# Kernel tuning notes

Hardware: AMD Instinct MI355X
Metric: run time of the kernel (lower is better)

Reference implementation:

```python
import jax, jax.numpy as jnp
import numpy as np

K = 4
HEADS = 4
IN_F = 128
OUT_F = 256
OUT_H = OUT_F // HEADS  # 64


def setup_inputs() -> dict:
    key = jax.random.key(0)
    ks = jax.random.split(key, 6)
    B, N = 8, 2048
    x = jax.random.normal(ks[0], (B, N, IN_F), dtype=jnp.float32)
    adj = jax.random.uniform(ks[1], (B, N, N), dtype=jnp.float32)
    # per-head linear: weight [H, out_h, in_f*(K+1)], bias [H, out_h]
    w_heads = 0.01 * jax.random.normal(ks[2], (HEADS, OUT_H, IN_F * (K + 1)), dtype=jnp.float32)
    b_heads = 0.01 * jax.random.normal(ks[3], (HEADS, OUT_H), dtype=jnp.float32)
    # final linear: [OUT_F, OUT_F]
    w_out = 0.01 * jax.random.normal(ks[4], (OUT_F, OUT_F), dtype=jnp.float32)
    b_out = 0.01 * jax.random.normal(ks[5], (OUT_F,), dtype=jnp.float32)
    return {"x": x, "adj": adj, "w_heads": w_heads, "b_heads": b_heads,
            "w_out": w_out, "b_out": b_out}


def _normalized_adj(adj):
    B, N, _ = adj.shape
    A_hat = adj + jnp.eye(N, dtype=adj.dtype)
    d = jnp.sum(A_hat, axis=2) ** -0.5          # [B, N]
    # L_hat = D^-1/2 A_hat D^-1/2 (diag scaling, no dense diag matmuls)
    return d[:, :, None] * A_hat * d[:, None, :]


def _legendre_stack(L, K):
    # elementwise Legendre recurrence on L; returns [B, N, N, K+1]
    P = [jnp.ones_like(L), L]
    for k in range(2, K + 1):
        P.append(((2 * k - 1) * L * P[-1] - (k - 1) * P[-2]) / k)
    return jnp.stack(P, axis=-1)


def reference(x, adj, w_heads, b_heads, w_out, b_out):
    B, N, F = x.shape
    L_hat = _normalized_adj(adj)                 # [B, N, N]
    LP = _legendre_stack(L_hat, K)               # [B, N, N, K+1] (shared by heads)
    # per-k propagation: cat([LP_k @ x for k], dim=2) -> k-major feature order
    prop = jnp.einsum('bnmk,bmf->bnkf', LP, x)   # [B, N, K+1, F]
    prop = prop.reshape(B, N, (K + 1) * F)       # [B, N, (K+1)*F]
    # per-head linear, concat heads along last dim (head-major)
    hout = jnp.einsum('bnc,hoc->bnho', prop, w_heads) + b_heads  # [B, N, H, out_h]
    hout = hout.reshape(B, N, HEADS * OUT_H)     # [B, N, OUT_F]
    return hout @ w_out.T + b_out                # [B, N, OUT_F]
```

## Files before the change

kernel.cpp:

```cpp
#include <hip/hip_runtime.h>
#include <hip/hip_bf16.h>
#include <stdint.h>

#define BATCH 8
#define NN    2048
#define FF    128
#define OUTF  256
#define C14   512

typedef unsigned short u16;
typedef u16  u16x8 __attribute__((ext_vector_type(8)));
typedef float f32x4 __attribute__((ext_vector_type(4)));

__device__ __forceinline__ u16 f2bf(float x) {
    union { float f; uint32_t u; } v; v.f = x;
    uint32_t r = v.u + 0x7FFFu + ((v.u >> 16) & 1u);
    return (u16)(r >> 16);
}
__device__ __forceinline__ uint32_t pk2(float a, float b) {
    __hip_bfloat162 h = __float22bfloat162_rn(make_float2(a, b));
    union { __hip_bfloat162 h; uint32_t u; } cv; cv.h = h; return cv.u;
}

__device__ __forceinline__ f32x4 mfma_bf16(u16x8 a, u16x8 b, f32x4 c) {
    asm("v_mfma_f32_16x16x32_bf16 %0, %1, %2, %0" : "+v"(c) : "v"(a), "v"(b));
    return c;
}

__global__ __launch_bounds__(256) void k_rowsum(const float* __restrict__ adj,
                                                float* __restrict__ dv) {
    size_t row = blockIdx.x;
    const float4* p = (const float4*)(adj + row * NN);
    int t = threadIdx.x;
    float4 v0 = p[t], v1 = p[t + 256];
    float s = v0.x + v0.y + v0.z + v0.w + v1.x + v1.y + v1.z + v1.w;
    #pragma unroll
    for (int off = 32; off > 0; off >>= 1) s += __shfl_down(s, off);
    __shared__ float r4[4];
    if ((t & 63) == 0) r4[t >> 6] = s;
    __syncthreads();
    if (t == 0) dv[row] = rsqrtf(r4[0] + r4[1] + r4[2] + r4[3] + 1.0f);
}

__global__ __launch_bounds__(256) void k_xprep(const float* __restrict__ x,
                                               u16* __restrict__ xT,
                                               float* __restrict__ part) {
    __shared__ u16 tile[FF][66];
    __shared__ float red[256];
    int b = blockIdx.x >> 5, mt = blockIdx.x & 31;
    const float* xb = x + ((size_t)(b * NN) + mt * 64) * FF;
    int t = threadIdx.x;
    float s = 0.f;
    #pragma unroll
    for (int i = 0; i < 32; ++i) {
        int idx = i * 256 + t;
        int ml = idx >> 7, f = idx & 127;
        float v = xb[idx];
        tile[f][ml] = f2bf(v);
        s += v;
    }
    red[t] = s;
    __syncthreads();
    u16* xb2 = xT + (size_t)b * FF * NN + mt * 64;
    #pragma unroll
    for (int i = 0; i < 16; ++i) {
        int p = i * 256 + t;
        int f = p >> 5, mp = p & 31;
        uint32_t v = (uint32_t)tile[f][2 * mp] | ((uint32_t)tile[f][2 * mp + 1] << 16);
        *(uint32_t*)(xb2 + (size_t)f * NN + 2 * mp) = v;
    }
    if (t < 128) part[(size_t)blockIdx.x * FF + t] = red[t] + red[t + 128];
}

__global__ __launch_bounds__(256) void k_weff(const float* __restrict__ wh,
                                              const float* __restrict__ wo,
                                              float* __restrict__ weff0,
                                              u16* __restrict__ w14) {
    int o = blockIdx.x, t = threadIdx.x;
    __shared__ float wrow[256];
    wrow[t] = wo[o * 256 + t];
    __syncthreads();
    int c2 = (t < 128) ? (t + 512) : 639;
    float s0 = 0.f, s1 = 0.f, s2 = 0.f;
    for (int i = 0; i < 256; ++i) {
        float w = wrow[i];
        const float* row = wh + (size_t)i * 640;
        s0 = fmaf(w, row[t], s0);
        s1 = fmaf(w, row[t + 256], s1);
        s2 = fmaf(w, row[c2], s2);
    }
    if (t < 128) weff0[o * 128 + t] = s0;
    else         w14[(size_t)o * C14 + (t - 128)] = f2bf(s0);
    w14[(size_t)o * C14 + (t + 128)] = f2bf(s1);
    if (t < 128) w14[(size_t)o * C14 + (t + 384)] = f2bf(s2);
}

__global__ __launch_bounds__(256) void k_cb(const float* __restrict__ part,
                                            const float* __restrict__ weff0,
                                            const float* __restrict__ wo,
                                            const float* __restrict__ bh,
                                            const float* __restrict__ bo,
                                            float* __restrict__ cb) {
    int b = blockIdx.x, t = threadIdx.x;
    __shared__ float cs[128];
    __shared__ float bhl[256];
    if (t < 128) {
        float s = 0.f;
        for (int j = 0; j < 32; ++j) s += part[(size_t)(b * 32 + j) * FF + t];
        cs[t] = s;
    }
    bhl[t] = bh[t];
    __syncthreads();
    float s = bo[t];
    for (int i = 0; i < 256; ++i) s = fmaf(wo[(size_t)t * 256 + i], bhl[i], s);
    for (int f = 0; f < 128; ++f) s = fmaf(weff0[t * 128 + f], cs[f], s);
    cb[b * 256 + t] = s;
}

struct MRegs { u16x8 bv[4]; f32x4 av[2]; f32x4 dmv; };

__device__ __forceinline__ void m_prefetch(MRegs& R, const u16* xTb, const float* adjb,
                                           const float* dvb, int mbase, int tid) {
    #pragma unroll
    for (int it = 0; it < 4; ++it) {
        int ci = it * 256 + tid; int f = ci >> 3, c = ci & 7;
        R.bv[it] = *(const u16x8*)(xTb + (size_t)f * NN + mbase + c * 8);
    }
    int q = tid & 15;
    R.dmv = *(const f32x4*)(dvb + mbase + q * 4);
    #pragma unroll
    for (int i = 0; i < 2; ++i) {
        int r = i * 16 + (tid >> 4);
        R.av[i] = *(const f32x4*)(adjb + (size_t)r * NN + mbase + q * 4);
    }
}

__device__ __forceinline__ void m_commit(const MRegs& R, u16* Ab, u16* Bb,
                                         const float* dn_l, int mbase, int rt, int tid) {
    #pragma unroll
    for (int it = 0; it < 4; ++it) {
        int ci = it * 256 + tid; int f = ci >> 3, c = ci & 7;
        *(u16x8*)((char*)Bb + f * 128 + ((c ^ (f & 7)) << 4)) = R.bv[it];
    }
    int q = tid & 15;
    #pragma unroll
    for (int i = 0; i < 2; ++i) {
        int r = i * 16 + (tid >> 4);
        int ng = rt * 32 + r - mbase - q * 4;
        float dnv = dn_l[r];
        float L[4], P2[4], P3[4], P4[4];
        #pragma unroll
        for (int j = 0; j < 4; ++j) {
            float a = R.av[i][j] + ((j == ng) ? 1.f : 0.f);
            L[j]  = a * dnv * R.dmv[j];
            P2[j] = fmaf(1.5f * L[j], L[j], -0.5f);
            P3[j] = L[j] * fmaf(1.66666667f, P2[j], -0.66666667f);
            P4[j] = fmaf(1.75f * L[j], P3[j], -0.75f * P2[j]);
        }
        char* base = (char*)Ab + (uint32_t)(r * 128 + ((q * 8) ^ ((r & 7) << 4)));
        *(uint2*)(base)         = make_uint2(pk2(L[0],  L[1]),  pk2(L[2],  L[3]));
        *(uint2*)(base + 4096)  = make_uint2(pk2(P2[0], P2[1]), pk2(P2[2], P2[3]));
        *(uint2*)(base + 8192)  = make_uint2(pk2(P3[0], P3[1]), pk2(P3[2], P3[3]));
        *(uint2*)(base + 12288) = make_uint2(pk2(P4[0], P4[1]), pk2(P4[2], P4[3]));
    }
}

__device__ __forceinline__ void m_mfma(const u16* A, const u16* B, int lane, f32x4 acc[2][8]) {
    #pragma unroll
    for (int kk = 0; kk < 2; ++kk) {
        int ch = (kk << 2) + (lane >> 4);
        u16x8 af[2];
        #pragma unroll
        for (int mi = 0; mi < 2; ++mi) {
            int row = mi * 16 + (lane & 15);
            af[mi] = *(const u16x8*)((const char*)A + row * 128 + ((ch ^ (row & 7)) << 4));
        }
        #pragma unroll
        for (int ni = 0; ni < 8; ++ni) {
            int fr = ni * 16 + (lane & 15);
            u16x8 bf = *(const u16x8*)((const char*)B + fr * 128 + ((ch ^ (fr & 7)) << 4));
            acc[0][ni] = mfma_bf16(af[0], bf, acc[0][ni]);
            acc[1][ni] = mfma_bf16(af[1], bf, acc[1][ni]);
        }
    }
}

__global__ __launch_bounds__(256, 2) void k_main(const float* __restrict__ adj,
                                                 const float* __restrict__ dvec,
                                                 const u16* __restrict__ xT,
                                                 u16* __restrict__ prop) {
    __shared__ __align__(16) u16 Abuf[2][4 * 32 * 64];
    __shared__ __align__(16) u16 Bbuf[2][FF * 64];
    __shared__ float dn_l[32];

    int tid = threadIdx.x, lane = tid & 63, wv = tid >> 6;
    int bb = blockIdx.x >> 6, rt = blockIdx.x & 63;
    const float* adjb = adj + (size_t)bb * NN * NN + (size_t)(rt * 32) * NN;
    const float* dvb = dvec + bb * NN;
    const u16* xTb = xT + (size_t)bb * FF * NN;

    f32x4 acc[2][8];
    #pragma unroll
    for (int mi = 0; mi < 2; ++mi)
        #pragma unroll
        for (int ni = 0; ni < 8; ++ni) acc[mi][ni] = (f32x4){0.f, 0.f, 0.f, 0.f};

    MRegs R0, R1;
    if (tid < 32) dn_l[tid] = dvec[bb * NN + rt * 32 + tid];
    m_prefetch(R0, xTb, adjb, dvb, 0, tid);
    __syncthreads();
    m_commit(R0, Abuf[0], Bbuf[0], dn_l, 0, rt, tid);
    m_prefetch(R1, xTb, adjb, dvb, 64, tid);
    __syncthreads();

    for (int ks = 0; ks < 32; ks += 2) {
        if (ks + 2 < 32) m_prefetch(R0, xTb, adjb, dvb, (ks + 2) * 64, tid);
        m_commit(R1, Abuf[1], Bbuf[1], dn_l, (ks + 1) * 64, rt, tid);
        m_mfma((const u16*)Abuf[0] + wv * 2048, (const u16*)Bbuf[0], lane, acc);
        __syncthreads();
        if (ks + 3 < 32) m_prefetch(R1, xTb, adjb, dvb, (ks + 3) * 64, tid);
        if (ks + 2 < 32) m_commit(R0, Abuf[0], Bbuf[0], dn_l, (ks + 2) * 64, rt, tid);
        m_mfma((const u16*)Abuf[1] + wv * 2048, (const u16*)Bbuf[1], lane, acc);
        __syncthreads();
    }
    asm volatile("s_nop 15\n\ts_nop 15");
    u16* pb = prop + ((size_t)bb * NN + rt * 32) * C14 + wv * 128;
    #pragma unroll
    for (int mi = 0; mi < 2; ++mi)
        #pragma unroll
        for (int ni = 0; ni < 8; ++ni) {
            int col = ni * 16 + (lane & 15);
            #pragma unroll
            for (int r4 = 0; r4 < 4; ++r4) {
                int row = mi * 16 + ((lane >> 4) << 2) + r4;
                pb[(size_t)row * C14 + col] = f2bf(acc[mi][ni][r4]);
            }
        }
}

struct FRegs { u16x8 a; u16x8 b[8]; };

__device__ __forceinline__ void f_prefetch(FRegs& R, const u16* Ap, const u16* w14,
                                           int mb, int tid) {
    { int r = tid >> 3, c = tid & 7;
      R.a = *(const u16x8*)(Ap + (size_t)r * C14 + mb + c * 8); }
    #pragma unroll
    for (int it = 0; it < 8; ++it) {
        int ci = it * 256 + tid; int o = ci >> 3, c = ci & 7;
        R.b[it] = *(const u16x8*)(w14 + (size_t)o * C14 + mb + c * 8);
    }
}
__device__ __forceinline__ void f_commit(const FRegs& R, u16* FA, u16* FB, int tid) {
    { int r = tid >> 3, c = tid & 7;
      *(u16x8*)((char*)FA + r * 128 + ((c ^ (r & 7)) << 4)) = R.a; }
    #pragma unroll
    for (int it = 0; it < 8; ++it) {
        int ci = it * 256 + tid; int o = ci >> 3, c = ci & 7;
        *(u16x8*)((char*)FB + o * 128 + ((c ^ (o & 7)) << 4)) = R.b[it];
    }
}
__device__ __forceinline__ void f_mfma(const u16* FA, const u16* FB, int lane, int wv,
                                       f32x4 acc[2][4]) {
    #pragma unroll
    for (int kk = 0; kk < 2; ++kk) {
        int ch = (kk << 2) + (lane >> 4);
        u16x8 af[2];
        #pragma unroll
        for (int mi = 0; mi < 2; ++mi) {
            int row = mi * 16 + (lane & 15);
            af[mi] = *(const u16x8*)((const char*)FA + row * 128 + ((ch ^ (row & 7)) << 4));
        }
        #pragma unroll
        for (int ni = 0; ni < 4; ++ni) {
            int o = wv * 64 + ni * 16 + (lane & 15);
            u16x8 bf = *(const u16x8*)((const char*)FB + o * 128 + ((ch ^ (o & 7)) << 4));
            acc[0][ni] = mfma_bf16(af[0], bf, acc[0][ni]);
            acc[1][ni] = mfma_bf16(af[1], bf, acc[1][ni]);
        }
    }
}

__global__ __launch_bounds__(256, 2) void k_final(const u16* __restrict__ prop,
                                                  const u16* __restrict__ w14,
                                                  const float* __restrict__ cb,
                                                  float* __restrict__ out) {
    __shared__ __align__(16) u16 FA[2][32 * 64];
    __shared__ __align__(16) u16 FB[2][256 * 64];
    int tid = threadIdx.x, lane = tid & 63, wv = tid >> 6;
    int rt = blockIdx.x, bb = rt >> 6;
    const u16* Ap = prop + (size_t)rt * 32 * C14;

    f32x4 acc[2][4];
    #pragma unroll
    for (int mi = 0; mi < 2; ++mi)
        #pragma unroll
        for (int ni = 0; ni < 4; ++ni) acc[mi][ni] = (f32x4){0.f, 0.f, 0.f, 0.f};

    FRegs R0, R1;
    f_prefetch(R0, Ap, w14, 0, tid);
    f_commit(R0, FA[0], FB[0], tid);
    f_prefetch(R1, Ap, w14, 64, tid);
    __syncthreads();

    for (int ks = 0; ks < 8; ks += 2) {
        if (ks + 2 < 8) f_prefetch(R0, Ap, w14, (ks + 2) * 64, tid);
        f_commit(R1, FA[1], FB[1], tid);
        f_mfma(FA[0], FB[0], lane, wv, acc);
        __syncthreads();
        if (ks + 3 < 8) f_prefetch(R1, Ap, w14, (ks + 3) * 64, tid);
        if (ks + 2 < 8) f_commit(R0, FA[0], FB[0], tid);
        f_mfma(FA[1], FB[1], lane, wv, acc);
        __syncthreads();
    }
    asm volatile("s_nop 15\n\ts_nop 15");
    float* ob = out + (size_t)rt * 32 * OUTF;
    const float* cbb = cb + bb * OUTF + wv * 64;
    #pragma unroll
    for (int mi = 0; mi < 2; ++mi)
        #pragma unroll
        for (int ni = 0; ni < 4; ++ni) {
            int col = ni * 16 + (lane & 15);
            float cv = cbb[col];
            #pragma unroll
            for (int r4 = 0; r4 < 4; ++r4) {
                int row = mi * 16 + ((lane >> 4) << 2) + r4;
                ob[(size_t)row * OUTF + wv * 64 + col] = acc[mi][ni][r4] + cv;
            }
        }
}

extern "C" void kernel_launch(void* const* d_in, const int* in_sizes, int n_in,
                              void* d_out, int out_size, void* d_ws, size_t ws_size,
                              hipStream_t stream) {
    const float* x   = (const float*)d_in[0];
    const float* adj = (const float*)d_in[1];
    const float* wh  = (const float*)d_in[2];
    const float* bh  = (const float*)d_in[3];
    const float* wo  = (const float*)d_in[4];
    const float* bo  = (const float*)d_in[5];

    char* p = (char*)d_ws;
    float* dvec  = (float*)p;  p += (size_t)BATCH * NN * 4;
    u16*   xT    = (u16*)p;    p += (size_t)BATCH * FF * NN * 2;
    float* part  = (float*)p;  p += (size_t)256 * FF * 4;
    float* weff0 = (float*)p;  p += (size_t)OUTF * FF * 4;
    u16*   w14   = (u16*)p;    p += (size_t)OUTF * C14 * 2;
    float* cbv   = (float*)p;  p += (size_t)BATCH * OUTF * 4;
    u16*   prop  = (u16*)p;    p += (size_t)BATCH * NN * C14 * 2;

    k_rowsum<<<dim3(BATCH * NN), dim3(256), 0, stream>>>(adj, dvec);
    k_xprep <<<dim3(256),        dim3(256), 0, stream>>>(x, xT, part);
    k_weff  <<<dim3(256),        dim3(256), 0, stream>>>(wh, wo, weff0, w14);
    k_cb    <<<dim3(BATCH),      dim3(256), 0, stream>>>(part, weff0, wo, bh, bo, cbv);
    k_main  <<<dim3(512),        dim3(256), 0, stream>>>(adj, dvec, xT, prop);
    k_final <<<dim3(512),        dim3(256), 0, stream>>>(prop, w14, cbv, (float*)d_out);
}
```

Measured before the change: 304.8 us.

## Fuse propagation and output GEMM kernels; merge x-prep and weight-fold kernels

Merges k_xprep and k_weff into one k_prep launch that splits work by block index. Fuses k_main and k_final into k_mf, so each block computes its 32-row propagation tile, writes it to a per-block scratch in global memory, then reads it back to run the output GEMM with the same shared-memory pool reused. This removes two launches and the gap between the propagation and final stages, and the reread tile is likely still in cache. The fused kernel's shared memory grows to 72KB, which could limit occupancy, and the intermediate still round-trips through global memory.

```diff
diff --git a/kernel.cpp b/kernel.cpp
--- a/kernel.cpp
+++ b/kernel.cpp
@@ -21,7 +21,6 @@
     __hip_bfloat162 h = __float22bfloat162_rn(make_float2(a, b));
     union { __hip_bfloat162 h; uint32_t u; } cv; cv.h = h; return cv.u;
 }
-
 __device__ __forceinline__ f32x4 mfma_bf16(u16x8 a, u16x8 b, f32x4 c) {
     asm("v_mfma_f32_16x16x32_bf16 %0, %1, %2, %0" : "+v"(c) : "v"(a), "v"(b));
     return c;
@@ -42,57 +41,57 @@
     if (t == 0) dv[row] = rsqrtf(r4[0] + r4[1] + r4[2] + r4[3] + 1.0f);
 }
 
-__global__ __launch_bounds__(256) void k_xprep(const float* __restrict__ x,
-                                               u16* __restrict__ xT,
-                                               float* __restrict__ part) {
-    __shared__ u16 tile[FF][66];
-    __shared__ float red[256];
-    int b = blockIdx.x >> 5, mt = blockIdx.x & 31;
-    const float* xb = x + ((size_t)(b * NN) + mt * 64) * FF;
-    int t = threadIdx.x;
-    float s = 0.f;
-    #pragma unroll
-    for (int i = 0; i < 32; ++i) {
-        int idx = i * 256 + t;
-        int ml = idx >> 7, f = idx & 127;
-        float v = xb[idx];
-        tile[f][ml] = f2bf(v);
-        s += v;
-    }
-    red[t] = s;
-    __syncthreads();
-    u16* xb2 = xT + (size_t)b * FF * NN + mt * 64;
-    #pragma unroll
-    for (int i = 0; i < 16; ++i) {
-        int p = i * 256 + t;
-        int f = p >> 5, mp = p & 31;
-        uint32_t v = (uint32_t)tile[f][2 * mp] | ((uint32_t)tile[f][2 * mp + 1] << 16);
-        *(uint32_t*)(xb2 + (size_t)f * NN + 2 * mp) = v;
-    }
-    if (t < 128) part[(size_t)blockIdx.x * FF + t] = red[t] + red[t + 128];
-}
-
-__global__ __launch_bounds__(256) void k_weff(const float* __restrict__ wh,
+__global__ __launch_bounds__(256) void k_prep(const float* __restrict__ x,
+                                              u16* __restrict__ xT,
+                                              float* __restrict__ part,
+                                              const float* __restrict__ wh,
                                               const float* __restrict__ wo,
                                               float* __restrict__ weff0,
                                               u16* __restrict__ w14) {
-    int o = blockIdx.x, t = threadIdx.x;
-    __shared__ float wrow[256];
-    wrow[t] = wo[o * 256 + t];
-    __syncthreads();
-    int c2 = (t < 128) ? (t + 512) : 639;
-    float s0 = 0.f, s1 = 0.f, s2 = 0.f;
-    for (int i = 0; i < 256; ++i) {
-        float w = wrow[i];
-        const float* row = wh + (size_t)i * 640;
-        s0 = fmaf(w, row[t], s0);
-        s1 = fmaf(w, row[t + 256], s1);
-        s2 = fmaf(w, row[c2], s2);
-    }
-    if (t < 128) weff0[o * 128 + t] = s0;
-    else         w14[(size_t)o * C14 + (t - 128)] = f2bf(s0);
-    w14[(size_t)o * C14 + (t + 128)] = f2bf(s1);
-    if (t < 128) w14[(size_t)o * C14 + (t + 384)] = f2bf(s2);
+    __shared__ u16 tile[FF][66];
+    __shared__ float red[256];
+    int t = threadIdx.x;
+    if (blockIdx.x < 256) {
+        int b = blockIdx.x >> 5, mt = blockIdx.x & 31;
+        const float* xb = x + ((size_t)(b * NN) + mt * 64) * FF;
+        float s = 0.f;
+        #pragma unroll
+        for (int i = 0; i < 32; ++i) {
+            int idx = i * 256 + t;
+            int ml = idx >> 7, f = idx & 127;
+            float v = xb[idx];
+            tile[f][ml] = f2bf(v);
+            s += v;
+        }
+        red[t] = s;
+        __syncthreads();
+        u16* xb2 = xT + (size_t)b * FF * NN + mt * 64;
+        #pragma unroll
+        for (int i = 0; i < 16; ++i) {
+            int p = i * 256 + t;
+            int f = p >> 5, mp = p & 31;
+            uint32_t v = (uint32_t)tile[f][2 * mp] | ((uint32_t)tile[f][2 * mp + 1] << 16);
+            *(uint32_t*)(xb2 + (size_t)f * NN + 2 * mp) = v;
+        }
+        if (t < 128) part[(size_t)blockIdx.x * FF + t] = red[t] + red[t + 128];
+    } else {
+        int o = blockIdx.x - 256;
+        red[t] = wo[o * 256 + t];
+        __syncthreads();
+        int c2 = (t < 128) ? (t + 512) : 639;
+        float s0 = 0.f, s1 = 0.f, s2 = 0.f;
+        for (int i = 0; i < 256; ++i) {
+            float w = red[i];
+            const float* row = wh + (size_t)i * 640;
+            s0 = fmaf(w, row[t], s0);
+            s1 = fmaf(w, row[t + 256], s1);
+            s2 = fmaf(w, row[c2], s2);
+        }
+        if (t < 128) weff0[o * 128 + t] = s0;
+        else         w14[(size_t)o * C14 + (t - 128)] = f2bf(s0);
+        w14[(size_t)o * C14 + (t + 128)] = f2bf(s1);
+        if (t < 128) w14[(size_t)o * C14 + (t + 384)] = f2bf(s2);
+    }
 }
 
 __global__ __launch_bounds__(256) void k_cb(const float* __restrict__ part,
@@ -135,12 +134,12 @@
     }
 }
 
-__device__ __forceinline__ void m_commit(const MRegs& R, u16* Ab, u16* Bb,
+__device__ __forceinline__ void m_commit(const MRegs& R, char* Ab, char* Bb,
                                          const float* dn_l, int mbase, int rt, int tid) {
     #pragma unroll
     for (int it = 0; it < 4; ++it) {
         int ci = it * 256 + tid; int f = ci >> 3, c = ci & 7;
-        *(u16x8*)((char*)Bb + f * 128 + ((c ^ (f & 7)) << 4)) = R.bv[it];
+        *(u16x8*)(Bb + f * 128 + ((c ^ (f & 7)) << 4)) = R.bv[it];
     }
     int q = tid & 15;
     #pragma unroll
@@ -157,7 +156,7 @@
             P3[j] = L[j] * fmaf(1.66666667f, P2[j], -0.66666667f);
             P4[j] = fmaf(1.75f * L[j], P3[j], -0.75f * P2[j]);
         }
-        char* base = (char*)Ab + (uint32_t)(r * 128 + ((q * 8) ^ ((r & 7) << 4)));
+        char* base = Ab + (uint32_t)(r * 128 + ((q * 8) ^ ((r & 7) << 4)));
         *(uint2*)(base)         = make_uint2(pk2(L[0],  L[1]),  pk2(L[2],  L[3]));
         *(uint2*)(base + 4096)  = make_uint2(pk2(P2[0], P2[1]), pk2(P2[2], P2[3]));
         *(uint2*)(base + 8192)  = make_uint2(pk2(P3[0], P3[1]), pk2(P3[2], P3[3]));
@@ -165,7 +164,7 @@
     }
 }
 
-__device__ __forceinline__ void m_mfma(const u16* A, const u16* B, int lane, f32x4 acc[2][8]) {
+__device__ __forceinline__ void m_mfma(const char* A, const char* B, int lane, f32x4 acc[2][8]) {
     #pragma unroll
     for (int kk = 0; kk < 2; ++kk) {
         int ch = (kk << 2) + (lane >> 4);
@@ -173,24 +172,68 @@
         #pragma unroll
         for (int mi = 0; mi < 2; ++mi) {
             int row = mi * 16 + (lane & 15);
-            af[mi] = *(const u16x8*)((const char*)A + row * 128 + ((ch ^ (row & 7)) << 4));
+            af[mi] = *(const u16x8*)(A + row * 128 + ((ch ^ (row & 7)) << 4));
         }
         #pragma unroll
         for (int ni = 0; ni < 8; ++ni) {
             int fr = ni * 16 + (lane & 15);
-            u16x8 bf = *(const u16x8*)((const char*)B + fr * 128 + ((ch ^ (fr & 7)) << 4));
+            u16x8 bf = *(const u16x8*)(B + fr * 128 + ((ch ^ (fr & 7)) << 4));
             acc[0][ni] = mfma_bf16(af[0], bf, acc[0][ni]);
             acc[1][ni] = mfma_bf16(af[1], bf, acc[1][ni]);
         }
     }
 }
 
-__global__ __launch_bounds__(256, 2) void k_main(const float* __restrict__ adj,
-                                                 const float* __restrict__ dvec,
-                                                 const u16* __restrict__ xT,
-                                                 u16* __restrict__ prop) {
-    __shared__ __align__(16) u16 Abuf[2][4 * 32 * 64];
-    __shared__ __align__(16) u16 Bbuf[2][FF * 64];
+struct FRegs { u16x8 a; u16x8 b[8]; };
+
+__device__ __forceinline__ void f_prefetch(FRegs& R, const u16* Ap, const u16* w14,
+                                           int mb, int tid) {
+    { int r = tid >> 3, c = tid & 7;
+      R.a = *(const u16x8*)(Ap + (size_t)r * C14 + mb + c * 8); }
+    #pragma unroll
+    for (int it = 0; it < 8; ++it) {
+        int ci = it * 256 + tid; int o = ci >> 3, c = ci & 7;
+        R.b[it] = *(const u16x8*)(w14 + (size_t)o * C14 + mb + c * 8);
+    }
+}
+__device__ __forceinline__ void f_commit(const FRegs& R, char* FA, char* FB, int tid) {
+    { int r = tid >> 3, c = tid & 7;
+      *(u16x8*)(FA + r * 128 + ((c ^ (r & 7)) << 4)) = R.a; }
+    #pragma unroll
+    for (int it = 0; it < 8; ++it) {
+        int ci = it * 256 + tid; int o = ci >> 3, c = ci & 7;
+        *(u16x8*)(FB + o * 128 + ((c ^ (o & 7)) << 4)) = R.b[it];
+    }
+}
+__device__ __forceinline__ void f_mfma(const char* FA, const char* FB, int lane, int wv,
+                                       f32x4 acc[2][4]) {
+    #pragma unroll
+    for (int kk = 0; kk < 2; ++kk) {
+        int ch = (kk << 2) + (lane >> 4);
+        u16x8 af[2];
+        #pragma unroll
+        for (int mi = 0; mi < 2; ++mi) {
+            int row = mi * 16 + (lane & 15);
+            af[mi] = *(const u16x8*)(FA + row * 128 + ((ch ^ (row & 7)) << 4));
+        }
+        #pragma unroll
+        for (int ni = 0; ni < 4; ++ni) {
+            int o = wv * 64 + ni * 16 + (lane & 15);
+            u16x8 bf = *(const u16x8*)(FB + o * 128 + ((ch ^ (o & 7)) << 4));
+            acc[0][ni] = mfma_bf16(af[0], bf, acc[0][ni]);
+            acc[1][ni] = mfma_bf16(af[1], bf, acc[1][ni]);
+        }
+    }
+}
+
+__global__ __launch_bounds__(256, 2) void k_mf(const float* __restrict__ adj,
+                                               const float* __restrict__ dvec,
+                                               const u16* __restrict__ xT,
+                                               const u16* __restrict__ w14,
+                                               const float* __restrict__ cb,
+                                               u16* __restrict__ propg,
+                                               float* __restrict__ out) {
+    __shared__ __align__(16) char pool[73728];
     __shared__ float dn_l[32];
 
     int tid = threadIdx.x, lane = tid & 63, wv = tid >> 6;
@@ -199,6 +242,9 @@
     const float* dvb = dvec + bb * NN;
     const u16* xTb = xT + (size_t)bb * FF * NN;
 
+    char* Ab0 = pool;            char* Ab1 = pool + 16384;
+    char* Bb0 = pool + 32768;    char* Bb1 = pool + 49152;
+
     f32x4 acc[2][8];
     #pragma unroll
     for (int mi = 0; mi < 2; ++mi)
@@ -209,22 +255,23 @@
     if (tid < 32) dn_l[tid] = dvec[bb * NN + rt * 32 + tid];
     m_prefetch(R0, xTb, adjb, dvb, 0, tid);
     __syncthreads();
-    m_commit(R0, Abuf[0], Bbuf[0], dn_l, 0, rt, tid);
+    m_commit(R0, Ab0, Bb0, dn_l, 0, rt, tid);
     m_prefetch(R1, xTb, adjb, dvb, 64, tid);
     __syncthreads();
 
     for (int ks = 0; ks < 32; ks += 2) {
         if (ks + 2 < 32) m_prefetch(R0, xTb, adjb, dvb, (ks + 2) * 64, tid);
-        m_commit(R1, Abuf[1], Bbuf[1], dn_l, (ks + 1) * 64, rt, tid);
-        m_mfma((const u16*)Abuf[0] + wv * 2048, (const u16*)Bbuf[0], lane, acc);
+        m_commit(R1, Ab1, Bb1, dn_l, (ks + 1) * 64, rt, tid);
+        m_mfma(Ab0 + (wv << 12), Bb0, lane, acc);
         __syncthreads();
         if (ks + 3 < 32) m_prefetch(R1, xTb, adjb, dvb, (ks + 3) * 64, tid);
-        if (ks + 2 < 32) m_commit(R0, Abuf[0], Bbuf[0], dn_l, (ks + 2) * 64, rt, tid);
-        m_mfma((const u16*)Abuf[1] + wv * 2048, (const u16*)Bbuf[1], lane, acc);
+        if (ks + 2 < 32) m_commit(R0, Ab0, Bb0, dn_l, (ks + 2) * 64, rt, tid);
+        m_mfma(Ab1 + (wv << 12), Bb1, lane, acc);
         __syncthreads();
     }
     asm volatile("s_nop 15\n\ts_nop 15");
-    u16* pb = prop + ((size_t)bb * NN + rt * 32) * C14 + wv * 128;
+
+    u16* pb = propg + (size_t)blockIdx.x * 32 * C14 + wv * 128;
     #pragma unroll
     for (int mi = 0; mi < 2; ++mi)
         #pragma unroll
@@ -236,84 +283,36 @@
                 pb[(size_t)row * C14 + col] = f2bf(acc[mi][ni][r4]);
             }
         }
-}
-
-struct FRegs { u16x8 a; u16x8 b[8]; };
-
-__device__ __forceinline__ void f_prefetch(FRegs& R, const u16* Ap, const u16* w14,
-                                           int mb, int tid) {
-    { int r = tid >> 3, c = tid & 7;
-      R.a = *(const u16x8*)(Ap + (size_t)r * C14 + mb + c * 8); }
-    #pragma unroll
-    for (int it = 0; it < 8; ++it) {
-        int ci = it * 256 + tid; int o = ci >> 3, c = ci & 7;
-        R.b[it] = *(const u16x8*)(w14 + (size_t)o * C14 + mb + c * 8);
-    }
-}
-__device__ __forceinline__ void f_commit(const FRegs& R, u16* FA, u16* FB, int tid) {
-    { int r = tid >> 3, c = tid & 7;
-      *(u16x8*)((char*)FA + r * 128 + ((c ^ (r & 7)) << 4)) = R.a; }
-    #pragma unroll
-    for (int it = 0; it < 8; ++it) {
-        int ci = it * 256 + tid; int o = ci >> 3, c = ci & 7;
-        *(u16x8*)((char*)FB + o * 128 + ((c ^ (o & 7)) << 4)) = R.b[it];
-    }
-}
-__device__ __forceinline__ void f_mfma(const u16* FA, const u16* FB, int lane, int wv,
-                                       f32x4 acc[2][4]) {
-    #pragma unroll
-    for (int kk = 0; kk < 2; ++kk) {
-        int ch = (kk << 2) + (lane >> 4);
-        u16x8 af[2];
-        #pragma unroll
-        for (int mi = 0; mi < 2; ++mi) {
-            int row = mi * 16 + (lane & 15);
-            af[mi] = *(const u16x8*)((const char*)FA + row * 128 + ((ch ^ (row & 7)) << 4));
-        }
-        #pragma unroll
-        for (int ni = 0; ni < 4; ++ni) {
-            int o = wv * 64 + ni * 16 + (lane & 15);
-            u16x8 bf = *(const u16x8*)((const char*)FB + o * 128 + ((ch ^ (o & 7)) << 4));
-            acc[0][ni] = mfma_bf16(af[0], bf, acc[0][ni]);
-            acc[1][ni] = mfma_bf16(af[1], bf, acc[1][ni]);
-        }
-    }
-}
-
-__global__ __launch_bounds__(256, 2) void k_final(const u16* __restrict__ prop,
-                                                  const u16* __restrict__ w14,
-                                                  const float* __restrict__ cb,
-                                                  float* __restrict__ out) {
-    __shared__ __align__(16) u16 FA[2][32 * 64];
-    __shared__ __align__(16) u16 FB[2][256 * 64];
-    int tid = threadIdx.x, lane = tid & 63, wv = tid >> 6;
-    int rt = blockIdx.x, bb = rt >> 6;
-    const u16* Ap = prop + (size_t)rt * 32 * C14;
-
-    f32x4 acc[2][4];
+    __syncthreads();
+
+    const u16* Ap = propg + (size_t)blockIdx.x * 32 * C14;
+    char* FA0 = pool;            char* FA1 = pool + 4096;
+    char* FB0 = pool + 8192;     char* FB1 = pool + 40960;
+
+    f32x4 facc[2][4];
     #pragma unroll
     for (int mi = 0; mi < 2; ++mi)
         #pragma unroll
-        for (int ni = 0; ni < 4; ++ni) acc[mi][ni] = (f32x4){0.f, 0.f, 0.f, 0.f};
-
-    FRegs R0, R1;
-    f_prefetch(R0, Ap, w14, 0, tid);
-    f_commit(R0, FA[0], FB[0], tid);
-    f_prefetch(R1, Ap, w14, 64, tid);
+        for (int ni = 0; ni < 4; ++ni) facc[mi][ni] = (f32x4){0.f, 0.f, 0.f, 0.f};
+
+    FRegs F0, F1;
+    f_prefetch(F0, Ap, w14, 0, tid);
+    f_commit(F0, FA0, FB0, tid);
+    f_prefetch(F1, Ap, w14, 64, tid);
     __syncthreads();
 
     for (int ks = 0; ks < 8; ks += 2) {
-        if (ks + 2 < 8) f_prefetch(R0, Ap, w14, (ks + 2) * 64, tid);
-        f_commit(R1, FA[1], FB[1], tid);
-        f_mfma(FA[0], FB[0], lane, wv, acc);
-        __syncthreads();
-        if (ks + 3 < 8) f_prefetch(R1, Ap, w14, (ks + 3) * 64, tid);
-        if (ks + 2 < 8) f_commit(R0, FA[0], FB[0], tid);
-        f_mfma(FA[1], FB[1], lane, wv, acc);
+        if (ks + 2 < 8) f_prefetch(F0, Ap, w14, (ks + 2) * 64, tid);
+        f_commit(F1, FA1, FB1, tid);
+        f_mfma(FA0, FB0, lane, wv, facc);
+        __syncthreads();
+        if (ks + 3 < 8) f_prefetch(F1, Ap, w14, (ks + 3) * 64, tid);
+        if (ks + 2 < 8) f_commit(F0, FA0, FB0, tid);
+        f_mfma(FA1, FB1, lane, wv, facc);
         __syncthreads();
     }
     asm volatile("s_nop 15\n\ts_nop 15");
-    float* ob = out + (size_t)rt * 32 * OUTF;
+    float* ob = out + ((size_t)bb * NN + rt * 32) * OUTF;
     const float* cbb = cb + bb * OUTF + wv * 64;
     #pragma unroll
     for (int mi = 0; mi < 2; ++mi)
@@ -324,7 +323,7 @@
             #pragma unroll
             for (int r4 = 0; r4 < 4; ++r4) {
                 int row = mi * 16 + ((lane >> 4) << 2) + r4;
-                ob[(size_t)row * OUTF + wv * 64 + col] = acc[mi][ni][r4] + cv;
+                ob[(size_t)row * OUTF + wv * 64 + col] = facc[mi][ni][r4] + cv;
             }
         }
 }
@@ -346,12 +345,10 @@
     float* weff0 = (float*)p;  p += (size_t)OUTF * FF * 4;
     u16*   w14   = (u16*)p;    p += (size_t)OUTF * C14 * 2;
     float* cbv   = (float*)p;  p += (size_t)BATCH * OUTF * 4;
-    u16*   prop  = (u16*)p;    p += (size_t)BATCH * NN * C14 * 2;
+    u16*   propg = (u16*)p;    p += (size_t)BATCH * NN * C14 * 2;
 
     k_rowsum<<<dim3(BATCH * NN), dim3(256), 0, stream>>>(adj, dvec);
-    k_xprep <<<dim3(256),        dim3(256), 0, stream>>>(x, xT, part);
-    k_weff  <<<dim3(256),        dim3(256), 0, stream>>>(wh, wo, weff0, w14);
+    k_prep  <<<dim3(512),        dim3(256), 0, stream>>>(x, xT, part, wh, wo, weff0, w14);
     k_cb    <<<dim3(BATCH),      dim3(256), 0, stream>>>(part, weff0, wo, bh, bo, cbv);
-    k_main  <<<dim3(512),        dim3(256), 0, stream>>>(adj, dvec, xT, prop);
-    k_final <<<dim3(512),        dim3(256), 0, stream>>>(prop, w14, cbv, (float*)d_out);
-}
+    k_mf    <<<dim3(512),        dim3(256), 0, stream>>>(adj, dvec, xT, w14, cbv, propg, (float*)d_out);
+}
```

Measured after the change: 300.7 us. About the same (-1.4%).
